# Performance work log

Measured on AMD Instinct MI355X. Metric: run time of the kernel, lower is better.

The kernel has to match this reference:

```python
import jax, jax.numpy as jnp
import numpy as np

B, L, C, H = 8, 16384, 128, 4
EPS = 1e-5


def setup_inputs() -> dict:
    key = jax.random.key(0)
    k1, k2, k3, k4 = jax.random.split(key, 4)
    return {
        "x": jax.random.normal(k1, (B, L, C), dtype=jnp.float32),
        "W_qkv": jax.random.normal(k2, (3 * C, C), dtype=jnp.float32) * (C ** -0.5),
        "W_out": jax.random.normal(k3, (C, C), dtype=jnp.float32) * (C ** -0.5),
        "b_out": jax.random.normal(k4, (C,), dtype=jnp.float32) * 0.01,
        "gn_w": jnp.ones((C,), dtype=jnp.float32),
        "gn_b": jnp.zeros((C,), dtype=jnp.float32),
    }


def reference(x, W_qkv, W_out, b_out, gn_w, gn_b):
    b, l, c = x.shape
    h = H
    d = c // h                      # dim_head
    scale = d ** -0.5
    xc = jnp.swapaxes(x, 1, 2)      # [b, c, l]
    # 1x1 conv == channel matmul
    qkv = jnp.einsum('oc,bcl->bol', W_qkv, xc)     # [b, 3c, l]
    q, k, v = jnp.split(qkv, 3, axis=1)
    q = q.reshape(b, h, d, l)
    k = k.reshape(b, h, d, l)
    v = v.reshape(b, h, d, l)
    q = jax.nn.softmax(q, axis=2) * scale          # softmax over head-dim
    k = jax.nn.softmax(k, axis=3)                  # softmax over length
    context = jnp.einsum('bhcj,bhdj->bhcd', k, v)  # [b, h, d, d]
    out = jnp.einsum('bhcd,bhdi->bhci', context, q)  # [b, h, d, l]
    out = out.reshape(b, h * d, l)
    out = jnp.einsum('oc,bcl->bol', W_out, out) + b_out[None, :, None]
    # GroupNorm(1, c): normalize over (channel, length) per sample
    mean = jnp.mean(out, axis=(1, 2), keepdims=True)
    var = jnp.var(out, axis=(1, 2), keepdims=True)
    out = (out - mean) * jax.lax.rsqrt(var + EPS)
    out = out * gn_w[None, :, None] + gn_b[None, :, None]
    return jnp.swapaxes(out, 1, 2)                 # [b, l, c]
```

## Files before the change

### kernel.cpp

```cpp
#include <hip/hip_runtime.h>

#define BATCH 8
#define SEQL 16384
#define NCH 128
#define NH 4
#define HD 32
#define GEPS 1e-5f

typedef __bf16 bf16x8 __attribute__((ext_vector_type(8)));
typedef __bf16 bf16x4 __attribute__((ext_vector_type(4)));
typedef float f32x4 __attribute__((ext_vector_type(4)));

#define WKV_B   0
#define WQ_B    65536
#define WO_B    98304
#define CTXB_B  131072
#define GNS_B   196608
#define CTXP_B  262144


__global__ void k_prep(const float* __restrict__ wqkv, const float* __restrict__ wout,
                       char* __restrict__ wsb) {
    int i = blockIdx.x * 256 + threadIdx.x;
    __bf16* wkvb = (__bf16*)(wsb + WKV_B);
    __bf16* wqb  = (__bf16*)(wsb + WQ_B);
    __bf16* wob  = (__bf16*)(wsb + WO_B);
    if (i < 384 * 128) {
        int o = i >> 7, c = i & 127;
        __bf16 v = (__bf16)wqkv[i];
        if (o < 128) wqb[o * 128 + c] = v;
        else         wkvb[(o - 128) * 128 + c] = v;
    }
    if (i < 128 * 128) wob[i] = (__bf16)wout[i];
    if (i < 16) ((float*)(wsb + GNS_B))[i] = 0.f;
}

__global__ __launch_bounds__(256, 3) void k_pass1(const float* __restrict__ x,
                                                  char* __restrict__ wsb, int P) {
    __shared__ __attribute__((aligned(16))) __bf16 xb[8352];
    __shared__ __attribute__((aligned(16))) __bf16 ekv[16464];
    const int t = threadIdx.x;
    const int lane = t & 63, wave = t >> 6;
    const int n16 = lane & 15, q = lane >> 4;
    const int batch = blockIdx.x / P, sub = blockIdx.x % P;
    const int nrep = 256 / P;
    const __bf16* __restrict__ wkvb = (const __bf16*)(wsb + WKV_B);

    bf16x8 aw[4][4];
#pragma unroll
    for (int mt = 0; mt < 4; mt++)
#pragma unroll
        for (int ks = 0; ks < 4; ks++)
            aw[mt][ks] = *(const bf16x8*)&wkvb[(wave * 64 + mt * 16 + n16) * 128 + ks * 32 + q * 8];

    f32x4 ctxacc[2][2];
#pragma unroll
    for (int i = 0; i < 2; i++)
#pragma unroll
        for (int j = 0; j < 2; j++) ctxacc[i][j] = (f32x4){0.f, 0.f, 0.f, 0.f};
    float zacc[4][4];
#pragma unroll
    for (int i = 0; i < 4; i++)
#pragma unroll
        for (int j = 0; j < 4; j++) zacc[i][j] = 0.f;

    {
        const float* xg = x + (size_t)(batch * SEQL + sub * 64) * NCH;
#pragma unroll
        for (int r = 0; r < 8; r++) {
            int e = t + r * 256;
            int tok = e >> 5, c4 = (e & 31) * 4;
            float4 v = ((const float4*)xg)[e];
            bf16x4 h; h.x = (__bf16)v.x; h.y = (__bf16)v.y; h.z = (__bf16)v.z; h.w = (__bf16)v.w;
            *(bf16x4*)&xb[(c4 >> 5) * 2088 + ((c4 >> 3) & 3) * 520 + tok * 8 + (c4 & 7)] = h;
        }
    }

    for (int rep = 0; rep < nrep; rep++) {
        __syncthreads();
#pragma unroll
        for (int half = 0; half < 2; half++) {
            f32x4 kvacc[4][2];
#pragma unroll
            for (int i = 0; i < 4; i++)
#pragma unroll
                for (int j = 0; j < 2; j++) kvacc[i][j] = (f32x4){0.f, 0.f, 0.f, 0.f};
#pragma unroll
            for (int ks = 0; ks < 4; ks++) {
                bf16x8 b[2];
#pragma unroll
                for (int nl = 0; nl < 2; nl++)
                    b[nl] = *(const bf16x8*)&xb[ks * 2088 + q * 520 + ((half * 2 + nl) * 16 + n16) * 8];
#pragma unroll
                for (int mt = 0; mt < 4; mt++)
#pragma unroll
                    for (int nl = 0; nl < 2; nl++)
                        kvacc[mt][nl] = __builtin_amdgcn_mfma_f32_16x16x32_bf16(
                            aw[mt][ks], b[nl], kvacc[mt][nl], 0, 0, 0);
            }
#pragma unroll
            for (int mt = 0; mt < 4; mt++)
#pragma unroll
                for (int nl = 0; nl < 2; nl++) {
                    int tt = (half * 2 + nl) * 16 + n16;
                    int base = (tt >> 5) * 8232 + ((tt >> 3) & 3) * 2056 + (tt & 7);
#pragma unroll
                    for (int r = 0; r < 4; r++) {
                        float vv = kvacc[mt][nl][r];
                        if (wave < 2) { vv = __expf(vv); zacc[mt][r] += vv; }
                        int o = wave * 64 + mt * 16 + q * 4 + r;
                        ekv[base + o * 8] = (__bf16)vv;
                    }
                }
        }
        float4 vpre[8];
        const bool hasNext = (rep + 1 < nrep);
        if (hasNext) {
            const float* xg2 = x + (size_t)(batch * SEQL + (sub + (rep + 1) * P) * 64) * NCH;
#pragma unroll
            for (int r = 0; r < 8; r++) vpre[r] = ((const float4*)xg2)[t + r * 256];
        }
        __syncthreads();
#pragma unroll
        for (int ks2 = 0; ks2 < 2; ks2++) {
            bf16x8 ea[2], vb[2];
#pragma unroll
            for (int ml = 0; ml < 2; ml++) {
                ea[ml] = *(const bf16x8*)&ekv[ks2 * 8232 + q * 2056 + (wave * 32 + ml * 16 + n16) * 8];
                vb[ml] = *(const bf16x8*)&ekv[ks2 * 8232 + q * 2056 + (128 + wave * 32 + ml * 16 + n16) * 8];
            }
#pragma unroll
            for (int ml = 0; ml < 2; ml++)
#pragma unroll
                for (int nl = 0; nl < 2; nl++)
                    ctxacc[ml][nl] = __builtin_amdgcn_mfma_f32_16x16x32_bf16(
                        ea[ml], vb[nl], ctxacc[ml][nl], 0, 0, 0);
        }
        if (hasNext) {
#pragma unroll
            for (int r = 0; r < 8; r++) {
                int e = t + r * 256;
                int tok = e >> 5, c4 = (e & 31) * 4;
                bf16x4 h;
                h.x = (__bf16)vpre[r].x; h.y = (__bf16)vpre[r].y;
                h.z = (__bf16)vpre[r].z; h.w = (__bf16)vpre[r].w;
                *(bf16x4*)&xb[(c4 >> 5) * 2088 + ((c4 >> 3) & 3) * 520 + tok * 8 + (c4 & 7)] = h;
            }
        }
    }

    float* ctxp = (float*)(wsb + CTXP_B) + (size_t)blockIdx.x * 4096 + wave * 1024;
#pragma unroll
    for (int nl = 0; nl < 2; nl++)
#pragma unroll
        for (int ml = 0; ml < 2; ml++) {
            float4 v4;
            v4.x = ctxacc[ml][nl][0]; v4.y = ctxacc[ml][nl][1];
            v4.z = ctxacc[ml][nl][2]; v4.w = ctxacc[ml][nl][3];
            *(float4*)&ctxp[(nl * 16 + n16) * 32 + ml * 16 + q * 4] = v4;
        }
    if (wave < 2) {
        float* zpT = (float*)(wsb + CTXP_B) + (size_t)BATCH * P * 4096;
#pragma unroll
        for (int mt = 0; mt < 4; mt++)
#pragma unroll
            for (int r = 0; r < 4; r++) {
                float z = zacc[mt][r];
                z += __shfl_xor(z, 1); z += __shfl_xor(z, 2);
                z += __shfl_xor(z, 4); z += __shfl_xor(z, 8);
                if (n16 == 0)
                    zpT[((size_t)batch * 128 + wave * 64 + mt * 16 + q * 4 + r) * P + sub] = z;
            }
    }
}

__global__ __launch_bounds__(256) void k_reduce(char* __restrict__ wsb, int P) {
    __shared__ float red[4][64];
    __shared__ float zw[32];
    const int tid = threadIdx.x;
    const int b = blockIdx.x >> 6, eg = blockIdx.x & 63;
    const float* ctxp = (const float*)(wsb + CTXP_B);
    const float* zpT = ctxp + (size_t)BATCH * P * 4096;

    {
        int ci = tid >> 3, pslot = tid & 7;
        size_t row = ((size_t)b * 128 + (size_t)(eg >> 4) * 32 + ci) * P;
        float zs = 0.f;
        for (int p = pslot; p < P; p += 8) zs += zpT[row + p];
        zs += __shfl_xor(zs, 1); zs += __shfl_xor(zs, 2); zs += __shfl_xor(zs, 4);
        if (pslot == 0) zw[ci] = zs;
    }
    {
        int pg = tid >> 6, e = tid & 63;
        int cnt = P >> 2;
        const float* base = ctxp + ((size_t)(b * P + pg * cnt)) * 4096 + eg * 64 + e;
        float cs = 0.f;
        for (int k = 0; k < cnt; k++) cs += base[(size_t)k * 4096];
        red[pg][e] = cs;
    }
    __syncthreads();
    if (tid < 64) {
        float tot = red[0][tid] + red[1][tid] + red[2][tid] + red[3][tid];
        int e = eg * 64 + tid;
        int h = e >> 10, d = (e >> 5) & 31, c = e & 31;
        ((__bf16*)(wsb + CTXB_B))[((size_t)b << 12) + (h << 10) + (c << 5) + d] =
            (__bf16)(tot / zw[c]);
    }
}

__global__ __launch_bounds__(256, 4) void k_pass2(const float* __restrict__ x,
                                                  const float* __restrict__ bout,
                                                  char* __restrict__ wsb,
                                                  float* __restrict__ out) {
    __shared__ __attribute__((aligned(16))) __bf16 xb[8352];
    __shared__ __attribute__((aligned(16))) __bf16 pB[8352];
    __shared__ float gred[8];
    const int t = threadIdx.x;
    const int lane = t & 63, wave = t >> 6;
    const int n16 = lane & 15, q = lane >> 4;
    const int batch = blockIdx.x >> 7, sub = blockIdx.x & 127;
    const __bf16* __restrict__ wqb = (const __bf16*)(wsb + WQ_B);
    const __bf16* __restrict__ wob = (const __bf16*)(wsb + WO_B);
    const __bf16* __restrict__ ctxb = (const __bf16*)(wsb + CTXB_B);

    bf16x8 actx[2];
#pragma unroll
    for (int ml = 0; ml < 2; ml++)
        actx[ml] = *(const bf16x8*)&ctxb[((size_t)(batch * 4 + wave) * 32 + ml * 16 + n16) * 32 + q * 8];
    float4 bias[2];
#pragma unroll
    for (int ml = 0; ml < 2; ml++)
        bias[ml] = *(const float4*)&bout[wave * 32 + ml * 16 + q * 4];

    {
        const float* xg = x + (size_t)(batch * SEQL + sub * 64) * NCH;
#pragma unroll
        for (int r = 0; r < 8; r++) {
            int e = t + r * 256;
            int tok = e >> 5, c4 = (e & 31) * 4;
            float4 v = ((const float4*)xg)[e];
            bf16x4 h; h.x = (__bf16)v.x; h.y = (__bf16)v.y; h.z = (__bf16)v.z; h.w = (__bf16)v.w;
            *(bf16x4*)&xb[(c4 >> 5) * 2088 + ((c4 >> 3) & 3) * 520 + tok * 8 + (c4 & 7)] = h;
        }
    }

    float s1 = 0.f, s2 = 0.f;
    bf16x4 hpre[8];

#pragma unroll
    for (int rep = 0; rep < 2; rep++) {
        const int chunk = sub + rep * 128;
        const size_t tok0 = (size_t)batch * SEQL + chunk * 64;
        __syncthreads();
        f32x4 qacc[2][4];
#pragma unroll
        for (int i = 0; i < 2; i++)
#pragma unroll
            for (int j = 0; j < 4; j++) qacc[i][j] = (f32x4){0.f, 0.f, 0.f, 0.f};
#pragma unroll
        for (int ks = 0; ks < 4; ks++) {
            bf16x8 aq_k[2];
#pragma unroll
            for (int ml = 0; ml < 2; ml++)
                aq_k[ml] = *(const bf16x8*)&wqb[(wave * 32 + ml * 16 + n16) * 128 + ks * 32 + q * 8];
            bf16x8 b[4];
#pragma unroll
            for (int nt = 0; nt < 4; nt++)
                b[nt] = *(const bf16x8*)&xb[ks * 2088 + q * 520 + (nt * 16 + n16) * 8];
#pragma unroll
            for (int ml = 0; ml < 2; ml++)
#pragma unroll
                for (int nt = 0; nt < 4; nt++)
                    qacc[ml][nt] = __builtin_amdgcn_mfma_f32_16x16x32_bf16(
                        aq_k[ml], b[nt], qacc[ml][nt], 0, 0, 0);
        }
        float4 vpre[8];
        if (rep == 0) {
            const float* xg2 = x + (size_t)(batch * SEQL + (sub + 128) * 64) * NCH;
#pragma unroll
            for (int r = 0; r < 8; r++) vpre[r] = ((const float4*)xg2)[t + r * 256];
        }
#pragma unroll
        for (int nt = 0; nt < 4; nt++) {
            float ss = 0.f;
#pragma unroll
            for (int ml = 0; ml < 2; ml++)
#pragma unroll
                for (int r = 0; r < 4; r++) {
                    float e = __expf(qacc[ml][nt][r]);
                    qacc[ml][nt][r] = e;
                    ss += e;
                }
            ss += __shfl_xor(ss, 16);
            ss += __shfl_xor(ss, 32);
            float inv = 0.17677669529663687f / ss;
#pragma unroll
            for (int ml = 0; ml < 2; ml++)
#pragma unroll
                for (int r = 0; r < 4; r++) qacc[ml][nt][r] *= inv;
        }
#pragma unroll
        for (int ml = 0; ml < 2; ml++)
#pragma unroll
            for (int nt = 0; nt < 4; nt++) {
                bf16x4 h;
                h.x = (__bf16)qacc[ml][nt][0]; h.y = (__bf16)qacc[ml][nt][1];
                h.z = (__bf16)qacc[ml][nt][2]; h.w = (__bf16)qacc[ml][nt][3];
                *(bf16x4*)&pB[wave * 2088 + (ml * 2 + (q >> 1)) * 520 +
                              (nt * 16 + n16) * 8 + (q & 1) * 4] = h;
            }
        __syncthreads();
        f32x4 aacc[2][4];
#pragma unroll
        for (int ml = 0; ml < 2; ml++)
#pragma unroll
            for (int nt = 0; nt < 4; nt++) {
                bf16x8 pb = *(const bf16x8*)&pB[wave * 2088 + q * 520 + (nt * 16 + n16) * 8];
                aacc[ml][nt] = __builtin_amdgcn_mfma_f32_16x16x32_bf16(
                    actx[ml], pb, (f32x4){0.f, 0.f, 0.f, 0.f}, 0, 0, 0);
            }
        if (rep == 0) {
#pragma unroll
            for (int r = 0; r < 8; r++) {
                bf16x4 h;
                h.x = (__bf16)vpre[r].x; h.y = (__bf16)vpre[r].y;
                h.z = (__bf16)vpre[r].z; h.w = (__bf16)vpre[r].w;
                hpre[r] = h;
            }
        }
        __bf16* attB = xb;
#pragma unroll
        for (int ml = 0; ml < 2; ml++)
#pragma unroll
            for (int nt = 0; nt < 4; nt++) {
                bf16x4 h;
                h.x = (__bf16)aacc[ml][nt][0]; h.y = (__bf16)aacc[ml][nt][1];
                h.z = (__bf16)aacc[ml][nt][2]; h.w = (__bf16)aacc[ml][nt][3];
                *(bf16x4*)&attB[wave * 2088 + (ml * 2 + (q >> 1)) * 520 +
                                (nt * 16 + n16) * 8 + (q & 1) * 4] = h;
            }
        __syncthreads();
        f32x4 oacc[2][4];
#pragma unroll
        for (int i = 0; i < 2; i++)
#pragma unroll
            for (int j = 0; j < 4; j++) oacc[i][j] = (f32x4){0.f, 0.f, 0.f, 0.f};
#pragma unroll
        for (int ks = 0; ks < 4; ks++) {
            bf16x8 ao_k[2];
#pragma unroll
            for (int ml = 0; ml < 2; ml++)
                ao_k[ml] = *(const bf16x8*)&wob[(wave * 32 + ml * 16 + n16) * 128 + ks * 32 + q * 8];
            bf16x8 b[4];
#pragma unroll
            for (int nt = 0; nt < 4; nt++)
                b[nt] = *(const bf16x8*)&attB[ks * 2088 + q * 520 + (nt * 16 + n16) * 8];
#pragma unroll
            for (int ml = 0; ml < 2; ml++)
#pragma unroll
                for (int nt = 0; nt < 4; nt++)
                    oacc[ml][nt] = __builtin_amdgcn_mfma_f32_16x16x32_bf16(
                        ao_k[ml], b[nt], oacc[ml][nt], 0, 0, 0);
        }
#pragma unroll
        for (int ml = 0; ml < 2; ml++)
#pragma unroll
            for (int nt = 0; nt < 4; nt++) {
                float4 vv;
                vv.x = oacc[ml][nt][0] + bias[ml].x;
                vv.y = oacc[ml][nt][1] + bias[ml].y;
                vv.z = oacc[ml][nt][2] + bias[ml].z;
                vv.w = oacc[ml][nt][3] + bias[ml].w;
                s1 += vv.x + vv.y + vv.z + vv.w;
                s2 += vv.x * vv.x + vv.y * vv.y + vv.z * vv.z + vv.w * vv.w;
                *(float4*)&out[(tok0 + nt * 16 + n16) * NCH + wave * 32 + ml * 16 + q * 4] = vv;
            }
        if (rep == 0) {
            __syncthreads();
#pragma unroll
            for (int r = 0; r < 8; r++) {
                int e = t + r * 256;
                int tok = e >> 5, c4 = (e & 31) * 4;
                *(bf16x4*)&xb[(c4 >> 5) * 2088 + ((c4 >> 3) & 3) * 520 + tok * 8 + (c4 & 7)] = hpre[r];
            }
        }
    }
#pragma unroll
    for (int off = 32; off > 0; off >>= 1) {
        s1 += __shfl_xor(s1, off);
        s2 += __shfl_xor(s2, off);
    }
    if (lane == 0) { gred[wave * 2 + 0] = s1; gred[wave * 2 + 1] = s2; }
    __syncthreads();
    if (t < 2) {
        float s = gred[t] + gred[2 + t] + gred[4 + t] + gred[6 + t];
        atomicAdd(&((float*)(wsb + GNS_B))[batch * 2 + t], s);
    }
}

__global__ __launch_bounds__(256) void k_gnorm(float* __restrict__ out,
                                               const char* __restrict__ wsb,
                                               const float* __restrict__ gw,
                                               const float* __restrict__ gb) {
    size_t base4 = ((size_t)blockIdx.x * 256 + threadIdx.x) * 2;
    int b = (int)(base4 >> 19);
    const float* gns = (const float*)(wsb + GNS_B);
    const float n = (float)NCH * (float)SEQL;
    float mean = gns[b * 2] / n;
    float var = gns[b * 2 + 1] / n - mean * mean;
    float rstd = rsqrtf(var + GEPS);
    int cbase = (int)((base4 & 31) * 4);
    float4 w0 = *(const float4*)&gw[cbase];
    float4 w1 = *(const float4*)&gw[cbase + 4];
    float4 b0 = *(const float4*)&gb[cbase];
    float4 b1 = *(const float4*)&gb[cbase + 4];
    float4 v0 = ((float4*)out)[base4];
    float4 v1 = ((float4*)out)[base4 + 1];
    v0.x = (v0.x - mean) * rstd * w0.x + b0.x;
    v0.y = (v0.y - mean) * rstd * w0.y + b0.y;
    v0.z = (v0.z - mean) * rstd * w0.z + b0.z;
    v0.w = (v0.w - mean) * rstd * w0.w + b0.w;
    v1.x = (v1.x - mean) * rstd * w1.x + b1.x;
    v1.y = (v1.y - mean) * rstd * w1.y + b1.y;
    v1.z = (v1.z - mean) * rstd * w1.z + b1.z;
    v1.w = (v1.w - mean) * rstd * w1.w + b1.w;
    ((float4*)out)[base4] = v0;
    ((float4*)out)[base4 + 1] = v1;
}

extern "C" void kernel_launch(void* const* d_in, const int* in_sizes, int n_in,
                              void* d_out, int out_size, void* d_ws, size_t ws_size,
                              hipStream_t stream) {
    const float* x    = (const float*)d_in[0];
    const float* wqkv = (const float*)d_in[1];
    const float* wout = (const float*)d_in[2];
    const float* bout = (const float*)d_in[3];
    const float* gw   = (const float*)d_in[4];
    const float* gb   = (const float*)d_in[5];
    float* out = (float*)d_out;
    char* wsb  = (char*)d_ws;

    int P = 128;
    while (P > 4 &&
           (size_t)CTXP_B + (size_t)BATCH * P * (16384 + 512) > ws_size)
        P >>= 1;

    k_prep<<<192, 256, 0, stream>>>(wqkv, wout, wsb);
    k_pass1<<<BATCH * P, 256, 0, stream>>>(x, wsb, P);
    k_reduce<<<BATCH * 64, 256, 0, stream>>>(wsb, P);
    k_pass2<<<1024, 256, 0, stream>>>(x, bout, wsb, out);
    k_gnorm<<<8192, 256, 0, stream>>>(out, wsb, gw, gb);
}
```

Measured before the change: 261.9 us.

## Raise pass1 occupancy: halve ekv LDS, reload weights per k-step, more blocks

The first-pass kernel no longer keeps the full K/V weight fragment in registers. It reloads the weights per k-step from global/L2 and halves the ekv shared buffer by consuming each 32-token half right after producing it. The output rows are reassigned so every wave computes exp for K rows, balancing the exp work across waves. Launch bounds go from 3 to 4 waves per SIMD and P doubles to 256, so each block handles one chunk and the x prefetch is dropped. The trade is more global weight loads and extra barriers in exchange for higher occupancy and more parallel blocks, which also doubles the partial-context writes and the reduction work.

Result: faster. 245.8 us (-6.1%).

```diff
diff --git a/kernel.cpp b/kernel.cpp
--- a/kernel.cpp
+++ b/kernel.cpp
@@ -35,10 +35,10 @@
     if (i < 16) ((float*)(wsb + GNS_B))[i] = 0.f;
 }
 
-__global__ __launch_bounds__(256, 3) void k_pass1(const float* __restrict__ x,
+__global__ __launch_bounds__(256, 4) void k_pass1(const float* __restrict__ x,
                                                   char* __restrict__ wsb, int P) {
     __shared__ __attribute__((aligned(16))) __bf16 xb[8352];
-    __shared__ __attribute__((aligned(16))) __bf16 ekv[16464];
+    __shared__ __attribute__((aligned(16))) __bf16 ekv[8232];
     const int t = threadIdx.x;
     const int lane = t & 63, wave = t >> 6;
     const int n16 = lane & 15, q = lane >> 4;
@@ -46,26 +46,20 @@
     const int nrep = 256 / P;
     const __bf16* __restrict__ wkvb = (const __bf16*)(wsb + WKV_B);
 
-    bf16x8 aw[4][4];
-#pragma unroll
-    for (int mt = 0; mt < 4; mt++)
-#pragma unroll
-        for (int ks = 0; ks < 4; ks++)
-            aw[mt][ks] = *(const bf16x8*)&wkvb[(wave * 64 + mt * 16 + n16) * 128 + ks * 32 + q * 8];
-
     f32x4 ctxacc[2][2];
 #pragma unroll
     for (int i = 0; i < 2; i++)
 #pragma unroll
         for (int j = 0; j < 2; j++) ctxacc[i][j] = (f32x4){0.f, 0.f, 0.f, 0.f};
-    float zacc[4][4];
-#pragma unroll
-    for (int i = 0; i < 4; i++)
+    float zacc[2][4];
+#pragma unroll
+    for (int i = 0; i < 2; i++)
 #pragma unroll
         for (int j = 0; j < 4; j++) zacc[i][j] = 0.f;
 
-    {
-        const float* xg = x + (size_t)(batch * SEQL + sub * 64) * NCH;
+    for (int rep = 0; rep < nrep; rep++) {
+        const int chunk = sub + rep * P;
+        const float* xg = x + (size_t)(batch * SEQL + chunk * 64) * NCH;
 #pragma unroll
         for (int r = 0; r < 8; r++) {
             int e = t + r * 256;
@@ -74,10 +68,8 @@
             bf16x4 h; h.x = (__bf16)v.x; h.y = (__bf16)v.y; h.z = (__bf16)v.z; h.w = (__bf16)v.w;
             *(bf16x4*)&xb[(c4 >> 5) * 2088 + ((c4 >> 3) & 3) * 520 + tok * 8 + (c4 & 7)] = h;
         }
-    }
-
-    for (int rep = 0; rep < nrep; rep++) {
         __syncthreads();
+
 #pragma unroll
         for (int half = 0; half < 2; half++) {
             f32x4 kvacc[4][2];
@@ -87,6 +79,10 @@
                 for (int j = 0; j < 2; j++) kvacc[i][j] = (f32x4){0.f, 0.f, 0.f, 0.f};
 #pragma unroll
             for (int ks = 0; ks < 4; ks++) {
+                bf16x8 aw_k[4];
+#pragma unroll
+                for (int mt = 0; mt < 4; mt++)
+                    aw_k[mt] = *(const bf16x8*)&wkvb[(mt * 64 + wave * 16 + n16) * 128 + ks * 32 + q * 8];
                 bf16x8 b[2];
 #pragma unroll
                 for (int nl = 0; nl < 2; nl++)
@@ -96,56 +92,38 @@
 #pragma unroll
                     for (int nl = 0; nl < 2; nl++)
                         kvacc[mt][nl] = __builtin_amdgcn_mfma_f32_16x16x32_bf16(
-                            aw[mt][ks], b[nl], kvacc[mt][nl], 0, 0, 0);
+                            aw_k[mt], b[nl], kvacc[mt][nl], 0, 0, 0);
             }
 #pragma unroll
             for (int mt = 0; mt < 4; mt++)
 #pragma unroll
                 for (int nl = 0; nl < 2; nl++) {
-                    int tt = (half * 2 + nl) * 16 + n16;
-                    int base = (tt >> 5) * 8232 + ((tt >> 3) & 3) * 2056 + (tt & 7);
+                    int ti = nl * 16 + n16;
+                    int base = (ti >> 3) * 2056 + (ti & 7);
 #pragma unroll
                     for (int r = 0; r < 4; r++) {
                         float vv = kvacc[mt][nl][r];
-                        if (wave < 2) { vv = __expf(vv); zacc[mt][r] += vv; }
-                        int o = wave * 64 + mt * 16 + q * 4 + r;
+                        if (mt < 2) { vv = __expf(vv); zacc[mt][r] += vv; }
+                        int o = mt * 64 + wave * 16 + q * 4 + r;
                         ekv[base + o * 8] = (__bf16)vv;
                     }
                 }
-        }
-        float4 vpre[8];
-        const bool hasNext = (rep + 1 < nrep);
-        if (hasNext) {
-            const float* xg2 = x + (size_t)(batch * SEQL + (sub + (rep + 1) * P) * 64) * NCH;
-#pragma unroll
-            for (int r = 0; r < 8; r++) vpre[r] = ((const float4*)xg2)[t + r * 256];
-        }
-        __syncthreads();
-#pragma unroll
-        for (int ks2 = 0; ks2 < 2; ks2++) {
-            bf16x8 ea[2], vb[2];
-#pragma unroll
-            for (int ml = 0; ml < 2; ml++) {
-                ea[ml] = *(const bf16x8*)&ekv[ks2 * 8232 + q * 2056 + (wave * 32 + ml * 16 + n16) * 8];
-                vb[ml] = *(const bf16x8*)&ekv[ks2 * 8232 + q * 2056 + (128 + wave * 32 + ml * 16 + n16) * 8];
-            }
-#pragma unroll
-            for (int ml = 0; ml < 2; ml++)
-#pragma unroll
-                for (int nl = 0; nl < 2; nl++)
-                    ctxacc[ml][nl] = __builtin_amdgcn_mfma_f32_16x16x32_bf16(
-                        ea[ml], vb[nl], ctxacc[ml][nl], 0, 0, 0);
-        }
-        if (hasNext) {
-#pragma unroll
-            for (int r = 0; r < 8; r++) {
-                int e = t + r * 256;
-                int tok = e >> 5, c4 = (e & 31) * 4;
-                bf16x4 h;
-                h.x = (__bf16)vpre[r].x; h.y = (__bf16)vpre[r].y;
-                h.z = (__bf16)vpre[r].z; h.w = (__bf16)vpre[r].w;
-                *(bf16x4*)&xb[(c4 >> 5) * 2088 + ((c4 >> 3) & 3) * 520 + tok * 8 + (c4 & 7)] = h;
-            }
+            __syncthreads();
+            {
+                bf16x8 ea[2], vb[2];
+#pragma unroll
+                for (int ml = 0; ml < 2; ml++) {
+                    ea[ml] = *(const bf16x8*)&ekv[q * 2056 + (wave * 32 + ml * 16 + n16) * 8];
+                    vb[ml] = *(const bf16x8*)&ekv[q * 2056 + (128 + wave * 32 + ml * 16 + n16) * 8];
+                }
+#pragma unroll
+                for (int ml = 0; ml < 2; ml++)
+#pragma unroll
+                    for (int nl = 0; nl < 2; nl++)
+                        ctxacc[ml][nl] = __builtin_amdgcn_mfma_f32_16x16x32_bf16(
+                            ea[ml], vb[nl], ctxacc[ml][nl], 0, 0, 0);
+            }
+            if (half == 0) __syncthreads();
         }
     }
 
@@ -159,17 +137,17 @@
             v4.z = ctxacc[ml][nl][2]; v4.w = ctxacc[ml][nl][3];
             *(float4*)&ctxp[(nl * 16 + n16) * 32 + ml * 16 + q * 4] = v4;
         }
-    if (wave < 2) {
+    {
         float* zpT = (float*)(wsb + CTXP_B) + (size_t)BATCH * P * 4096;
 #pragma unroll
-        for (int mt = 0; mt < 4; mt++)
+        for (int mt = 0; mt < 2; mt++)
 #pragma unroll
             for (int r = 0; r < 4; r++) {
                 float z = zacc[mt][r];
                 z += __shfl_xor(z, 1); z += __shfl_xor(z, 2);
                 z += __shfl_xor(z, 4); z += __shfl_xor(z, 8);
                 if (n16 == 0)
-                    zpT[((size_t)batch * 128 + wave * 64 + mt * 16 + q * 4 + r) * P + sub] = z;
+                    zpT[((size_t)batch * 128 + mt * 64 + wave * 16 + q * 4 + r) * P + sub] = z;
             }
     }
 }
@@ -440,7 +418,7 @@
     float* out = (float*)d_out;
     char* wsb  = (char*)d_ws;
 
-    int P = 128;
+    int P = 256;
     while (P > 4 &&
            (size_t)CTXP_B + (size_t)BATCH * P * (16384 + 512) > ws_size)
         P >>= 1;
```
